# Kernel tuning notes

Measured on AMD Instinct MI355X. Metric: run time of the kernel, lower is better.

## Reference

```python
import jax, jax.numpy as jnp
import numpy as np


def _pe_2d(H, W, C, dtype):
    # PositionalEncodingPermute2D: returns (C, H, W)
    ch_half = (C + 1) // 2
    inv = 1.0 / (10000.0 ** (jnp.arange(0, ch_half, 2, dtype=jnp.float32) / ch_half))
    tH = jnp.arange(H, dtype=jnp.float32)
    tW = jnp.arange(W, dtype=jnp.float32)
    sinH = tH[:, None] * inv[None, :]              # (H, ch_half//2)
    sinW = tW[:, None] * inv[None, :]              # (W, ch_half//2)
    embH = jnp.concatenate([jnp.sin(sinH), jnp.cos(sinH)], axis=-1)  # (H, ch_half)
    embW = jnp.concatenate([jnp.sin(sinW), jnp.cos(sinW)], axis=-1)  # (W, ch_half)
    E = jnp.concatenate([
        jnp.broadcast_to(embW[None, :, :], (H, W, ch_half)),
        jnp.broadcast_to(embH[:, None, :], (H, W, ch_half)),
    ], axis=-1)[..., :C]                            # (H, W, C)
    return jnp.transpose(E, (2, 0, 1)).astype(dtype)  # (C, H, W)


def setup_inputs() -> dict:
    key = jax.random.key(0)
    k0, k1, k2, k3 = jax.random.split(key, 4)
    B, C, H, W = 4, 256, 64, 64
    s = 1.0 / np.sqrt(C)  # kaiming-ish scale
    return {
        "x": jax.random.normal(k0, (B, C, H, W), dtype=jnp.float32),
        "wq": jax.random.normal(k1, (C, C), dtype=jnp.float32) * s,
        "wk": jax.random.normal(k2, (C, C), dtype=jnp.float32) * s,
        "wv": jax.random.normal(k3, (C, C), dtype=jnp.float32) * s,
    }


def reference(x, wq, wk, wv):
    B, C, H, W = x.shape
    scale = C ** (-0.5)
    x = x + _pe_2d(H, W, C, x.dtype)[None]          # (B, C, H, W)
    X = x.reshape(B, C, H * W).transpose(0, 2, 1)   # (B, N, C)
    Q = jnp.einsum('bnc,dc->bnd', X, wq)
    K = jnp.einsum('bnc,dc->bnd', X, wk)
    V = jnp.einsum('bnc,dc->bnd', X, wv)
    A = jax.nn.softmax(jnp.einsum('bnd,bmd->bnm', Q, K) * scale, axis=-1)
    Y = jnp.einsum('bnm,bmd->bnd', A, V)            # (B, N, C)
    return Y.transpose(0, 2, 1).reshape(B, C, H, W)
```

## Files before the change

### kernel.cpp

```cpp
#include <hip/hip_runtime.h>
#include <hip/hip_bf16.h>

#define BB 4
#define CC 256
#define NN 4096
#define NSPLIT 4
#define KSPLIT (NN / NSPLIT)
#define NT (KSPLIT / 32)

typedef __attribute__((ext_vector_type(8))) short short8;
typedef __attribute__((ext_vector_type(4))) float floatx4;
typedef __attribute__((ext_vector_type(4))) unsigned short ushortx4;

__device__ __forceinline__ float bf2f(unsigned short u) {
  union { unsigned int i; float f; } cv; cv.i = ((unsigned int)u) << 16; return cv.f;
}
__device__ __forceinline__ unsigned short f2bf(float f) {
  union { __hip_bfloat16 h; unsigned short u; } cv; cv.h = __float2bfloat16(f); return cv.u;
}
__device__ __forceinline__ unsigned int cvtpk_bf16(float lo, float hi) {
  unsigned int r;
  asm("v_cvt_pk_bf16_f32 %0, %1, %2" : "=v"(r) : "v"(lo), "v"(hi));
  return r;
}

#define MFMA(a, b, c) __builtin_amdgcn_mfma_f32_16x16x32_bf16((a), (b), (c), 0, 0, 0)

__device__ __forceinline__ void dma16(const unsigned short* g, unsigned short* l) {
  __builtin_amdgcn_global_load_lds(
      (const __attribute__((address_space(1))) unsigned int*)g,
      (__attribute__((address_space(3))) unsigned int*)l, 16, 0, 0);
}
#define S_BARRIER __builtin_amdgcn_s_barrier()
#define MEMFENCE __asm__ volatile("" ::: "memory")
#define SCHED_FENCE __builtin_amdgcn_sched_barrier(0)

__global__ __launch_bounds__(256) void wcvt(const float* __restrict__ w0,
                                            const float* __restrict__ w1,
                                            const float* __restrict__ w2,
                                            unsigned short* __restrict__ o0,
                                            unsigned short* __restrict__ o1,
                                            unsigned short* __restrict__ o2,
                                            float* __restrict__ PEt) {
  if (blockIdx.y == 3) {
    int idx = blockIdx.x * 256 + threadIdx.x;
    int c = idx >> 6, p = idx & 63, j = c & 63;
    float freq = exp2f(-0.2076205059304601f * (float)j);
    float arg = (float)p * freq;
    PEt[idx] = (c & 64) ? cosf(arg) : sinf(arg);
    return;
  }
  const float* w = (blockIdx.y == 0) ? w0 : (blockIdx.y == 1) ? w1 : w2;
  unsigned short* o = (blockIdx.y == 0) ? o0 : (blockIdx.y == 1) ? o1 : o2;
  float s = (blockIdx.y == 0) ? 0.0901684400555590f : 1.0f;
  int i = (blockIdx.x * 256 + threadIdx.x) * 4;
  floatx4 v = *(const floatx4*)&w[i];
  ushortx4 p;
#pragma unroll
  for (int r = 0; r < 4; r++) p[r] = f2bf(v[r] * s);
  *(ushortx4*)&o[i] = p;
}

__global__ __launch_bounds__(256) void prep_x(const float* __restrict__ x,
                                              const float* __restrict__ PEt,
                                              unsigned short* __restrict__ Xbf) {
  __shared__ float tile[32][33];
  int b = blockIdx.z;
  int n0 = blockIdx.x * 32, c0 = blockIdx.y * 32;
  int tx = threadIdx.x, ty = threadIdx.y;
#pragma unroll
  for (int i = 0; i < 4; i++) {
    int c = c0 + ty + i * 8;
    int n = n0 + tx;
    float v = x[((long)(b * CC + c)) * NN + n];
    int hh = n >> 6, ww = n & 63;
    v += PEt[(c << 6) | ((c < 128) ? ww : hh)];
    tile[ty + i * 8][tx] = v;
  }
  __syncthreads();
#pragma unroll
  for (int i = 0; i < 4; i++) {
    int n = n0 + ty + i * 8;
    int c = c0 + tx;
    Xbf[((long)(b * NN + n)) * CC + c] = f2bf(tile[tx][ty + i * 8]);
  }
}

__global__ __launch_bounds__(256, 2) void gemm_fused(const unsigned short* __restrict__ Xbf,
                                                     const unsigned short* __restrict__ Wqk,
                                                     const unsigned short* __restrict__ Wv,
                                                     unsigned short* __restrict__ QK,
                                                     unsigned short* __restrict__ Vt) {
  __shared__ alignas(16) unsigned short Af[2][8 * 512];
  __shared__ alignas(16) unsigned short Bf[2][8 * 512];
  const unsigned short *Ab, *Bb;
  unsigned short* Ob;
  long row0, col0;
  int ldo;
  int F = blockIdx.x;
  if (F < 512) {
    int b = F >> 7, r = F & 127;
    row0 = (long)(r >> 2) * 128;
    col0 = (long)(r & 3) * 128;
    Ab = Xbf + (long)b * NN * CC;
    Bb = Wqk;
    Ob = QK + (long)b * NN * 512;
    ldo = 512;
  } else {
    int F2 = F - 512;
    int b = F2 >> 6, r = F2 & 63;
    row0 = (long)(r >> 5) * 128;
    col0 = (long)(r & 31) * 128;
    Ab = Wv;
    Bb = Xbf + (long)b * NN * CC;
    Ob = Vt + (long)b * CC * NN;
    ldo = NN;
  }
  int t = threadIdx.x, wave = t >> 6, lane = t & 63, quad = lane >> 4, l15 = lane & 15;
  int wr = wave >> 1, wc = wave & 1;

  auto stage = [&](int k0, int buf) {
#pragma unroll
    for (int i = 0; i < 2; i++) {
      int fg = wave * 2 + i;
      dma16(&Ab[(row0 + fg * 16 + l15) * 256 + k0 + quad * 8], &Af[buf][fg * 512]);
      dma16(&Bb[(col0 + fg * 16 + l15) * 256 + k0 + quad * 8], &Bf[buf][fg * 512]);
    }
  };

  floatx4 acc[4][4] = {};
  stage(0, 0);
  MEMFENCE;
#pragma unroll
  for (int ki = 0; ki < 8; ki++) {
    int buf = ki & 1;
    S_BARRIER;
    MEMFENCE;
    if (ki + 1 < 8) {
      stage((ki + 1) * 32, buf ^ 1);
      MEMFENCE;
      __builtin_amdgcn_s_waitcnt(0xF74);
    } else {
      __builtin_amdgcn_s_waitcnt(0xF70);
    }
    S_BARRIER;
    MEMFENCE;
    short8 af[4], bf[4];
#pragma unroll
    for (int i = 0; i < 4; i++) {
      af[i] = *(const short8*)&Af[buf][(wr * 4 + i) * 512 + lane * 8];
      bf[i] = *(const short8*)&Bf[buf][(wc * 4 + i) * 512 + lane * 8];
    }
#pragma unroll
    for (int i = 0; i < 4; i++)
#pragma unroll
      for (int j = 0; j < 4; j++) acc[i][j] = MFMA(af[i], bf[j], acc[i][j]);
  }

#pragma unroll
  for (int i = 0; i < 4; i++)
#pragma unroll
    for (int j = 0; j < 4; j++) {
      long col = col0 + (wc * 4 + j) * 16 + l15;
#pragma unroll
      for (int r = 0; r < 4; r++) {
        long row = row0 + (wr * 4 + i) * 16 + quad * 4 + r;
        Ob[row * (long)ldo + col] = f2bf(acc[i][j][r]);
      }
    }
}

__global__ __launch_bounds__(256, 2) void attn(const unsigned short* __restrict__ QKg,
                                               const unsigned short* __restrict__ Vtg,
                                               unsigned short* __restrict__ Opart,
                                               float* __restrict__ Lp) {
  __shared__ alignas(16) unsigned short Kl[2 * 8192];
  __shared__ alignas(16) unsigned short Vl[2 * 8192];
  int F = blockIdx.x;
  int c = F >> 5, qt = F & 31;
  int sp = c & 3, b = c >> 2;
  long q0 = (long)qt * 128;
  int t = threadIdx.x, wave = t >> 6, lane = t & 63, quad = lane >> 4, l15 = lane & 15;
  const unsigned short* Qb = QKg + (long)b * NN * 512;
  const unsigned short* Kb = Qb + 256;
  const unsigned short* Vb = Vtg + (long)b * CC * NN;

  short8 qf[2][8];
#pragma unroll
  for (int qb = 0; qb < 2; qb++) {
    long qrow = q0 + wave * 32 + qb * 16 + l15;
#pragma unroll
    for (int ks = 0; ks < 8; ks++)
      qf[qb][ks] = *(const short8*)&Qb[qrow * 512 + ks * 32 + quad * 8];
  }

  floatx4 acc[2][16] = {};
  float rs[2] = {0.f, 0.f};

  const int idx0 = (((lane >> 4) & 1) << 7) | ((lane & 15) << 2);
  const int idx1 = idx0 + 64;
  const bool lo32 = lane < 32;

  const int kbeg = sp * KSPLIT;

  auto stageT = [&](int tt) {
    int m0 = kbeg + tt * 32;
    int kb = (tt & 1) * 8192;
#pragma unroll
    for (int st = 0; st < 2; st++) {
#pragma unroll
      for (int i = 0; i < 2; i++) {
        int d = wave * 2 + i;
        int fg = st * 8 + d;
        dma16(&Kb[(long)(m0 + st * 16 + l15) * 512 + d * 32 + quad * 8],
              &Kl[kb + fg * 512]);
        dma16(&Vb[(long)(fg * 16 + l15) * NN + m0 + quad * 8],
              &Vl[kb + fg * 512]);
      }
    }
  };

  MEMFENCE;
  __builtin_amdgcn_s_waitcnt(0x070);
  SCHED_FENCE;
  MEMFENCE;
  stageT(0);
  MEMFENCE;

#pragma unroll 1
  for (int tt = 0; tt < NT; tt++) {
    S_BARRIER;
    MEMFENCE;
    SCHED_FENCE;
    if (tt + 1 < NT) {
      stageT(tt + 1);
      MEMFENCE;
      __builtin_amdgcn_s_waitcnt(0xF78);
    } else {
      __builtin_amdgcn_s_waitcnt(0xF70);
    }
    SCHED_FENCE;
    S_BARRIER;
    MEMFENCE;
    SCHED_FENCE;

    int kb = (tt & 1) * 8192;

    floatx4 s2[2][2];
    {
      floatx4 z = {0.f, 0.f, 0.f, 0.f};
      s2[0][0] = z; s2[0][1] = z; s2[1][0] = z; s2[1][1] = z;
    }
    __builtin_amdgcn_s_setprio(1);
#pragma unroll
    for (int fgk = 0; fgk < 16; fgk++) {
      short8 kf = *(const short8*)&Kl[kb + fgk * 512 + lane * 8];
      int mt = fgk >> 3, ks = fgk & 7;
      s2[0][mt] = MFMA(kf, qf[0][ks], s2[0][mt]);
      s2[1][mt] = MFMA(kf, qf[1][ks], s2[1][mt]);
    }
    __builtin_amdgcn_s_setprio(0);

    unsigned int pw[2][2][2];
#pragma unroll
    for (int qb = 0; qb < 2; qb++)
#pragma unroll
      for (int mt = 0; mt < 2; mt++) {
        float e0 = __builtin_amdgcn_exp2f(s2[qb][mt][0]);
        float e1 = __builtin_amdgcn_exp2f(s2[qb][mt][1]);
        float e2 = __builtin_amdgcn_exp2f(s2[qb][mt][2]);
        float e3 = __builtin_amdgcn_exp2f(s2[qb][mt][3]);
        rs[qb] += (e0 + e1) + (e2 + e3);
        pw[qb][mt][0] = cvtpk_bf16(e0, e1);
        pw[qb][mt][1] = cvtpk_bf16(e2, e3);
      }

    short8 pf[2];
#pragma unroll
    for (int qb = 0; qb < 2; qb++) {
      unsigned int x0 = (unsigned int)__builtin_amdgcn_ds_bpermute(idx0, (int)pw[qb][0][0]);
      unsigned int y0 = (unsigned int)__builtin_amdgcn_ds_bpermute(idx0, (int)pw[qb][1][0]);
      unsigned int x1 = (unsigned int)__builtin_amdgcn_ds_bpermute(idx0, (int)pw[qb][0][1]);
      unsigned int y1 = (unsigned int)__builtin_amdgcn_ds_bpermute(idx0, (int)pw[qb][1][1]);
      unsigned int x2 = (unsigned int)__builtin_amdgcn_ds_bpermute(idx1, (int)pw[qb][0][0]);
      unsigned int y2 = (unsigned int)__builtin_amdgcn_ds_bpermute(idx1, (int)pw[qb][1][0]);
      unsigned int x3 = (unsigned int)__builtin_amdgcn_ds_bpermute(idx1, (int)pw[qb][0][1]);
      unsigned int y3 = (unsigned int)__builtin_amdgcn_ds_bpermute(idx1, (int)pw[qb][1][1]);
      union { unsigned int u[4]; short8 s; } pk;
      pk.u[0] = lo32 ? x0 : y0;
      pk.u[1] = lo32 ? x1 : y1;
      pk.u[2] = lo32 ? x2 : y2;
      pk.u[3] = lo32 ? x3 : y3;
      pf[qb] = pk.s;
    }

    __builtin_amdgcn_s_setprio(1);
#pragma unroll
    for (int db = 0; db < 16; db++) {
      short8 vf = *(const short8*)&Vl[kb + db * 512 + lane * 8];
      acc[0][db] = MFMA(pf[0], vf, acc[0][db]);
      acc[1][db] = MFMA(pf[1], vf, acc[1][db]);
    }
    __builtin_amdgcn_s_setprio(0);
  }

  unsigned short* Ob = Opart + (long)(b * NSPLIT + sp) * CC * NN;
#pragma unroll
  for (int qb = 0; qb < 2; qb++) {
    long nidx = q0 + wave * 32 + qb * 16 + quad * 4;
#pragma unroll
    for (int db = 0; db < 16; db++) {
      long d = db * 16 + l15;
      ushortx4 pk;
#pragma unroll
      for (int r = 0; r < 4; r++) pk[r] = f2bf(acc[qb][db][r]);
      *(ushortx4*)&Ob[d * NN + nidx] = pk;
    }
    float v = rs[qb];
    v += __shfl_xor(v, 16, 64);
    v += __shfl_xor(v, 32, 64);
    if (quad == 0)
      Lp[(long)(b * NSPLIT + sp) * NN + q0 + wave * 32 + qb * 16 + l15] = v;
  }
}

__global__ __launch_bounds__(256) void combine(const unsigned short* __restrict__ Op,
                                               const float* __restrict__ Lp,
                                               float* __restrict__ Out) {
  __shared__ float Wl[64];
  int b = blockIdx.z;
  int d0 = blockIdx.y * 64, n0 = blockIdx.x * 64;
  int t = threadIdx.x;
  if (t < 64) {
    int n = n0 + t;
    float L = 0.f;
#pragma unroll
    for (int s = 0; s < NSPLIT; s++) L += Lp[(long)(b * NSPLIT + s) * NN + n];
    Wl[t] = 1.0f / L;
  }
  __syncthreads();
  int tn = t & 15, td = t >> 4;
  int nb = n0 + tn * 4;
  float w[4];
#pragma unroll
  for (int r = 0; r < 4; r++) w[r] = Wl[tn * 4 + r];
#pragma unroll
  for (int dd = 0; dd < 4; dd++) {
    int d = d0 + td * 4 + dd;
    floatx4 o = {0.f, 0.f, 0.f, 0.f};
#pragma unroll
    for (int s = 0; s < NSPLIT; s++) {
      ushortx4 pv = *(const ushortx4*)&Op[((long)(b * NSPLIT + s) * CC + d) * NN + nb];
#pragma unroll
      for (int r = 0; r < 4; r++) o[r] += bf2f(pv[r]);
    }
#pragma unroll
    for (int r = 0; r < 4; r++) o[r] *= w[r];
    *(floatx4*)&Out[((long)b * CC + d) * NN + nb] = o;
  }
}

extern "C" void kernel_launch(void* const* d_in, const int* in_sizes, int n_in,
                              void* d_out, int out_size, void* d_ws, size_t ws_size,
                              hipStream_t stream) {
  const float* x = (const float*)d_in[0];
  const float* wq = (const float*)d_in[1];
  const float* wk = (const float*)d_in[2];
  const float* wv = (const float*)d_in[3];
  float* out = (float*)d_out;

  char* ws = (char*)d_ws;
  unsigned short* QKbuf = (unsigned short*)(ws);
  unsigned short* Vt = (unsigned short*)(ws + (16l << 20));
  unsigned short* Xbf = (unsigned short*)(ws + (24l << 20));
  unsigned short* Opart = (unsigned short*)(ws + (24l << 20));
  float* Lp = (float*)(ws + (56l << 20));
  unsigned short* Wqk = (unsigned short*)(ws + (57l << 20));
  unsigned short* Wv = (unsigned short*)(ws + (57l << 20) + (1 << 19));
  float* PEt = (float*)(ws + (57l << 20) + (3 << 18));

  wcvt<<<dim3(CC * CC / 1024, 4), 256, 0, stream>>>(wq, wk, wv, Wqk, Wqk + CC * CC, Wv, PEt);
  prep_x<<<dim3(NN / 32, CC / 32, BB), dim3(32, 8), 0, stream>>>(x, PEt, Xbf);
  gemm_fused<<<dim3(768), 256, 0, stream>>>(Xbf, Wqk, Wv, QKbuf, Vt);
  attn<<<dim3(512), 256, 0, stream>>>(QKbuf, Vt, Opart, Lp);
  combine<<<dim3(NN / 64, CC / 64, BB), 256, 0, stream>>>(Opart, Lp, out);
}
```

Measured before the change: 189.8 us.

## Software-pipeline attention loop so PV of previous tile overlaps QK of current tile

```diff
diff --git a/kernel.cpp b/kernel.cpp
--- a/kernel.cpp
+++ b/kernel.cpp
@@ -203,7 +203,7 @@
 
   const int kbeg = sp * KSPLIT;
 
-  auto stageT = [&](int tt) {
+  auto stageK = [&](int tt) {
     int m0 = kbeg + tt * 32;
     int kb = (tt & 1) * 8192;
 #pragma unroll
@@ -214,38 +214,24 @@
         int fg = st * 8 + d;
         dma16(&Kb[(long)(m0 + st * 16 + l15) * 512 + d * 32 + quad * 8],
               &Kl[kb + fg * 512]);
+      }
+    }
+  };
+  auto stageV = [&](int tt) {
+    int m0 = kbeg + tt * 32;
+    int kb = (tt & 1) * 8192;
+#pragma unroll
+    for (int st = 0; st < 2; st++) {
+#pragma unroll
+      for (int i = 0; i < 2; i++) {
+        int fg = st * 8 + wave * 2 + i;
         dma16(&Vb[(long)(fg * 16 + l15) * NN + m0 + quad * 8],
               &Vl[kb + fg * 512]);
       }
     }
   };
 
-  MEMFENCE;
-  __builtin_amdgcn_s_waitcnt(0x070);
-  SCHED_FENCE;
-  MEMFENCE;
-  stageT(0);
-  MEMFENCE;
-
-#pragma unroll 1
-  for (int tt = 0; tt < NT; tt++) {
-    S_BARRIER;
-    MEMFENCE;
-    SCHED_FENCE;
-    if (tt + 1 < NT) {
-      stageT(tt + 1);
-      MEMFENCE;
-      __builtin_amdgcn_s_waitcnt(0xF78);
-    } else {
-      __builtin_amdgcn_s_waitcnt(0xF70);
-    }
-    SCHED_FENCE;
-    S_BARRIER;
-    MEMFENCE;
-    SCHED_FENCE;
-
-    int kb = (tt & 1) * 8192;
-
+  auto qk_sm = [&](int kb, short8 (&pfo)[2]) {
     floatx4 s2[2][2];
     {
       floatx4 z = {0.f, 0.f, 0.f, 0.f};
@@ -275,7 +261,6 @@
         pw[qb][mt][1] = cvtpk_bf16(e2, e3);
       }
 
-    short8 pf[2];
 #pragma unroll
     for (int qb = 0; qb < 2; qb++) {
       unsigned int x0 = (unsigned int)__builtin_amdgcn_ds_bpermute(idx0, (int)pw[qb][0][0]);
@@ -291,18 +276,74 @@
       pk.u[1] = lo32 ? x1 : y1;
       pk.u[2] = lo32 ? x2 : y2;
       pk.u[3] = lo32 ? x3 : y3;
-      pf[qb] = pk.s;
-    }
-
+      pfo[qb] = pk.s;
+    }
+  };
+
+  auto pv = [&](int kb, short8 (&pfi)[2]) {
     __builtin_amdgcn_s_setprio(1);
 #pragma unroll
     for (int db = 0; db < 16; db++) {
       short8 vf = *(const short8*)&Vl[kb + db * 512 + lane * 8];
-      acc[0][db] = MFMA(pf[0], vf, acc[0][db]);
-      acc[1][db] = MFMA(pf[1], vf, acc[1][db]);
+      acc[0][db] = MFMA(pfi[0], vf, acc[0][db]);
+      acc[1][db] = MFMA(pfi[1], vf, acc[1][db]);
     }
     __builtin_amdgcn_s_setprio(0);
-  }
+  };
+
+  auto region = [&](int t_, short8 (&pfp)[2], short8 (&pfc)[2]) {
+    S_BARRIER;
+    MEMFENCE;
+    SCHED_FENCE;
+    if (t_ + 1 < NT) stageK(t_ + 1);
+    stageV(t_);
+    MEMFENCE;
+    if (t_ + 1 < NT)
+      __builtin_amdgcn_s_waitcnt(0xF78);
+    else
+      __builtin_amdgcn_s_waitcnt(0xF74);
+    SCHED_FENCE;
+    S_BARRIER;
+    MEMFENCE;
+    SCHED_FENCE;
+    pv(((t_ - 1) & 1) * 8192, pfp);
+    qk_sm((t_ & 1) * 8192, pfc);
+  };
+
+  MEMFENCE;
+  __builtin_amdgcn_s_waitcnt(0x070);
+  SCHED_FENCE;
+  MEMFENCE;
+  stageK(0);
+  MEMFENCE;
+  S_BARRIER;
+  MEMFENCE;
+  SCHED_FENCE;
+  stageK(1);
+  stageV(0);
+  MEMFENCE;
+  __builtin_amdgcn_s_waitcnt(0xF78);
+  SCHED_FENCE;
+  S_BARRIER;
+  MEMFENCE;
+  SCHED_FENCE;
+  short8 pfA[2], pfB[2];
+  qk_sm(0, pfA);
+
+#pragma unroll 1
+  for (int t2 = 1; t2 + 1 < NT; t2 += 2) {
+    region(t2, pfA, pfB);
+    region(t2 + 1, pfB, pfA);
+  }
+  region(NT - 1, pfA, pfB);
+
+  MEMFENCE;
+  __builtin_amdgcn_s_waitcnt(0xF70);
+  SCHED_FENCE;
+  S_BARRIER;
+  MEMFENCE;
+  SCHED_FENCE;
+  pv(((NT - 1) & 1) * 8192, pfB);
 
   unsigned short* Ob = Opart + (long)(b * NSPLIT + sp) * CC * NN;
 #pragma unroll
```

After: 201.1 us. 5.9% more time.
